# Optimization experiments

Hardware: AMD Instinct MI355X
Metric: run time of the kernel (lower is better)

Reference implementation:

```python
import jax, jax.numpy as jnp
import numpy as np

B, S, H = 4, 2048, 1024
NH, HD = 16, 64  # num heads, head dim
SCALE = 1.0 / np.sqrt(HD).astype(np.float32)
CLAMP = 1e9
EPS = 1e-9

def setup_inputs() -> dict:
    key = jax.random.key(0)
    ks = jax.random.split(key, 4)
    w_std = 0.02
    return {
        "hidden_states": jax.random.normal(ks[0], (B, S, H), dtype=jnp.float32),
        "Wq": jax.random.normal(ks[1], (H, H), dtype=jnp.float32) * w_std,
        "bq": jnp.zeros((H,), dtype=jnp.float32),
        "Wk": jax.random.normal(ks[2], (H, H), dtype=jnp.float32) * w_std,
        "bk": jnp.zeros((H,), dtype=jnp.float32),
        "Wv": jax.random.normal(ks[3], (H, H), dtype=jnp.float32) * w_std,
        "bv": jnp.zeros((H,), dtype=jnp.float32),
    }

def reference(hidden_states, Wq, bq, Wk, bk, Wv, bv):
    b, s, h = hidden_states.shape
    # linear projections, then split heads: [B,S,H] -> [B,S,NH,HD]
    q = (hidden_states @ Wq + bq).reshape(b, s, NH, HD)
    k = (hidden_states @ Wk + bk).reshape(b, s, NH, HD)
    v = (hidden_states @ Wv + bv).reshape(b, s, NH, HD)
    # scores: [B,NH,Sq,Sk]
    scores = jnp.einsum("bqhd,bkhd->bhqk", q, k) * SCALE
    scores = jnp.clip(scores, -CLAMP, CLAMP)
    probs = jax.nn.softmax(scores, axis=-1) + EPS
    # dropout: eval mode (identity)
    ctx = jnp.einsum("bhqk,bkhd->bqhd", probs, v)
    return ctx.reshape(b, s, h)
```

## Files before the change

### kernel.cpp

```cpp
#include <hip/hip_runtime.h>
#include <hip/hip_bf16.h>
#include <stdint.h>

#define B_ 4
#define S_ 2048
#define H_ 1024
#define NH_ 16
#define HD_ 64
#define SCALE_ 0.125f
#define LOG2E_ 1.4426950408889634f

typedef __bf16 bf16x8 __attribute__((ext_vector_type(8)));
typedef float f32x4 __attribute__((ext_vector_type(4)));
typedef unsigned short us4 __attribute__((ext_vector_type(4)));
typedef unsigned short us8 __attribute__((ext_vector_type(8)));
typedef unsigned short ushort_t;

__device__ __forceinline__ ushort_t f2bf(float f) {
  union { float f; uint32_t u; } a; a.f = f;
  uint32_t r = (a.u + 0x7fffu + ((a.u >> 16) & 1u)) >> 16;
  return (ushort_t)r;
}

__device__ __forceinline__ void async16(const void* g, void* l) {
  __builtin_amdgcn_global_load_lds(
      (const __attribute__((address_space(1))) unsigned int*)(uintptr_t)g,
      (__attribute__((address_space(3))) unsigned int*)(uintptr_t)l, 16, 0, 0);
}

__global__ __launch_bounds__(256) void conv_x(const float4* __restrict__ x,
                                              ushort_t* __restrict__ xb) {
  int i = blockIdx.x * 256 + threadIdx.x;
  float4 v = x[i];
  us4 o;
  o.x = f2bf(v.x); o.y = f2bf(v.y); o.z = f2bf(v.z); o.w = f2bf(v.w);
  *(us4*)(xb + (size_t)i * 4) = o;
}

__global__ __launch_bounds__(256) void conv_w(const float* __restrict__ Wq,
                                              const float* __restrict__ Wk,
                                              const float* __restrict__ Wv,
                                              ushort_t* __restrict__ Wt) {
  __shared__ __align__(16) ushort_t T[64 * 64];
  int bid = blockIdx.x;
  int w = bid >> 8;
  int t2 = bid & 255;
  int kt = (t2 >> 4) * 64, nt = (t2 & 15) * 64;
  const float* W = (w == 0) ? Wq : (w == 1) ? Wk : Wv;
  int tid = threadIdx.x;
  int k = tid >> 2, nq = tid & 3;
#pragma unroll
  for (int j4 = 0; j4 < 4; ++j4) {
    int n = nq * 4 + j4 * 16;
    float4 f = *(const float4*)(W + (size_t)(kt + k) * H_ + nt + n);
    us4 o;
    o.x = f2bf(f.x); o.y = f2bf(f.y); o.z = f2bf(f.z); o.w = f2bf(f.w);
    *(us4*)(T + k * 64 + (((n >> 3) ^ (k & 7)) * 8) + (n & 7)) = o;
  }
  __syncthreads();
  int n2 = tid >> 2, kq = tid & 3;
  us8 o0, o1;
#pragma unroll
  for (int j = 0; j < 16; ++j) {
    int kk = kq * 16 + j;
    ushort_t v = T[kk * 64 + (((n2 >> 3) ^ (kk & 7)) * 8) + (n2 & 7)];
    if (j < 8) o0[j] = v; else o1[j - 8] = v;
  }
  size_t obase = (size_t)w * (H_ * H_) + (size_t)(nt + n2) * H_ + kt + kq * 16;
  *(us8*)(Wt + obase) = o0;
  *(us8*)(Wt + obase + 8) = o1;
}

__global__ __launch_bounds__(256) void qkv_gemm(const ushort_t* __restrict__ Xb,
                                                const ushort_t* __restrict__ Wt,
                                                const float* __restrict__ bq,
                                                const float* __restrict__ bk,
                                                const float* __restrict__ bv,
                                                ushort_t* __restrict__ QKV) {
  __shared__ __align__(16) ushort_t As[128 * 32];
  __shared__ __align__(16) ushort_t Bs[128 * 32];
  int nb = blockIdx.x;
  int mb = blockIdx.y;
  int w = nb >> 3;
  int n_base = (nb & 7) * 128;
  int m_base = mb * 128;
  const ushort_t* Wtw = Wt + (size_t)w * (H_ * H_);
  int tid = threadIdx.x;
  int lane = tid & 63, wave = tid >> 6;
  int wr = wave >> 1, wc = wave & 1;
  int g = lane >> 4, l15 = lane & 15;

  f32x4 acc[4][4];
#pragma unroll
  for (int i = 0; i < 4; i++)
#pragma unroll
    for (int j = 0; j < 4; j++) acc[i][j] = (f32x4){0.f, 0.f, 0.f, 0.f};

  for (int kt = 0; kt < 32; ++kt) {
    int k0 = kt * 32;
    __syncthreads();
#pragma unroll
    for (int it = 0; it < 2; ++it) {
      int chunk = tid + it * 256;
      int r = chunk >> 2, c = chunk & 3;
      async16(Xb + (size_t)(m_base + r) * H_ + k0 + c * 8, As + chunk * 8);
      async16(Wtw + (size_t)(n_base + r) * H_ + k0 + c * 8, Bs + chunk * 8);
    }
    __builtin_amdgcn_s_waitcnt(0);
    __syncthreads();

    bf16x8 af[4], bf[4];
#pragma unroll
    for (int mi = 0; mi < 4; mi++)
      af[mi] = *(const bf16x8*)(As + (wr * 64 + mi * 16 + l15) * 32 + g * 8);
#pragma unroll
    for (int ni = 0; ni < 4; ni++)
      bf[ni] = *(const bf16x8*)(Bs + (wc * 64 + ni * 16 + l15) * 32 + g * 8);
#pragma unroll
    for (int mi = 0; mi < 4; mi++)
#pragma unroll
      for (int ni = 0; ni < 4; ni++)
        acc[mi][ni] = __builtin_amdgcn_mfma_f32_16x16x32_bf16(af[mi], bf[ni], acc[mi][ni], 0, 0, 0);
  }

  const float* bias = (w == 0) ? bq : (w == 1) ? bk : bv;
  float mult = (w == 0) ? SCALE_ * LOG2E_ : 1.0f;
  ushort_t* out = QKV + (size_t)w * (8192u * 1024u);
#pragma unroll
  for (int ni = 0; ni < 4; ++ni) {
    int n_col = n_base + wc * 64 + ni * 16 + l15;
    float bb = bias[n_col];
#pragma unroll
    for (int mi = 0; mi < 4; ++mi) {
      int m_row = m_base + wr * 64 + mi * 16 + g * 4;
#pragma unroll
      for (int reg = 0; reg < 4; ++reg) {
        float v = (acc[mi][ni][reg] + bb) * mult;
        out[(size_t)(m_row + reg) * H_ + n_col] = f2bf(v);
      }
    }
  }
}

__global__ __launch_bounds__(256) void transpose_v(const ushort_t* __restrict__ V,
                                                   ushort_t* __restrict__ Vt) {
  __shared__ __align__(16) ushort_t T[64 * 64];
  int st = blockIdx.x;
  int bh = blockIdx.y;
  int b = bh >> 4, h = bh & 15;
  int tid = threadIdx.x;
  int r = tid >> 3, c8 = tid & 7;
#pragma unroll
  for (int it = 0; it < 2; ++it) {
    int s = it * 32 + r;
    us8 v = *(const us8*)(V + (size_t)(b * S_ + st * 64 + s) * H_ + h * HD_ + c8 * 8);
    *(us8*)(T + s * 64 + ((c8 ^ ((s >> 3) & 7)) * 8)) = v;
  }
  __syncthreads();
#pragma unroll
  for (int it = 0; it < 2; ++it) {
    int d = it * 32 + r;
    us8 o;
#pragma unroll
    for (int j = 0; j < 8; ++j) {
      int s = c8 * 8 + j;
      o[j] = T[s * 64 + (((d >> 3) ^ c8) * 8) + (d & 7)];
    }
    *(us8*)(Vt + (size_t)(bh * 64 + d) * S_ + st * 64 + c8 * 8) = o;
  }
}

__global__ __launch_bounds__(512) void attn(const ushort_t* __restrict__ QKV,
                                            const ushort_t* __restrict__ Vt,
                                            float* __restrict__ out) {
  __shared__ __align__(16) ushort_t Ks[2][64 * 64];
  __shared__ __align__(16) ushort_t Vs[2][64 * 64];
  __shared__ __align__(16) ushort_t Ps[8][32 * 64];
  int qt = blockIdx.x;
  int bh = blockIdx.y;
  int b = bh >> 4, h = bh & 15;
  int tid = threadIdx.x, lane = tid & 63, wave = tid >> 6;
  int g = lane >> 4, l15 = lane & 15;

  const ushort_t* Qb = QKV;
  const ushort_t* Kb = QKV + 8388608u;

  bf16x8 qf[2][2];
#pragma unroll
  for (int mi = 0; mi < 2; ++mi) {
    int q_row = qt * 256 + wave * 32 + mi * 16 + l15;
    size_t qoff = (size_t)(b * S_ + q_row) * H_ + h * HD_;
    qf[mi][0] = *(const bf16x8*)(Qb + qoff + g * 8);
    qf[mi][1] = *(const bf16x8*)(Qb + qoff + 32 + g * 8);
  }

  f32x4 of[2][4], lsum[2];
#pragma unroll
  for (int mi = 0; mi < 2; mi++) {
    lsum[mi] = (f32x4){0.f, 0.f, 0.f, 0.f};
#pragma unroll
    for (int ni = 0; ni < 4; ni++) of[mi][ni] = (f32x4){0.f, 0.f, 0.f, 0.f};
  }

  union { us8 u; bf16x8 b; } uo;
#pragma unroll
  for (int j = 0; j < 8; ++j) uo.u[j] = 0x3F80;
  bf16x8 ones = uo.b;

  ushort_t* Pw = Ps[wave];
  int swz = l15 & 7;

  int s0 = tid >> 3;
  int cg0 = (tid & 7) ^ (s0 & 7);
  const ushort_t* srcK = Kb + (size_t)(b * S_ + s0) * H_ + h * HD_ + cg0 * 8;
  const ushort_t* srcV = Vt + ((size_t)bh * 64 + s0) * S_ + cg0 * 8;

  async16(srcK, Ks[0] + tid * 8);
  async16(srcV, Vs[0] + tid * 8);

#pragma unroll 2
  for (int kb = 0; kb < 32; ++kb) {
    int cur = kb & 1, nxt = cur ^ 1;
    __syncthreads();
    if (kb < 31) {
      async16(srcK + (size_t)(kb + 1) * 64 * H_, Ks[nxt] + tid * 8);
      async16(srcV + (size_t)(kb + 1) * 64, Vs[nxt] + tid * 8);
      __builtin_amdgcn_s_waitcnt(0xF72);
    } else {
      __builtin_amdgcn_s_waitcnt(0xF70);
    }
    __syncthreads();
    const ushort_t* Kc = Ks[cur];
    const ushort_t* Vc = Vs[cur];

#pragma unroll
    for (int c = 0; c < 4; ++c) {
      int row = c * 16 + l15;
      bf16x8 k0 = *(const bf16x8*)(Kc + row * 64 + ((g ^ (row & 7)) * 8));
      bf16x8 k1 = *(const bf16x8*)(Kc + row * 64 + (((4 + g) ^ (row & 7)) * 8));
#pragma unroll
      for (int mi = 0; mi < 2; ++mi) {
        f32x4 s = (f32x4){0.f, 0.f, 0.f, 0.f};
        s = __builtin_amdgcn_mfma_f32_16x16x32_bf16(k0, qf[mi][0], s, 0, 0, 0);
        s = __builtin_amdgcn_mfma_f32_16x16x32_bf16(k1, qf[mi][1], s, 0, 0, 0);
        us4 pk;
#pragma unroll
        for (int r = 0; r < 4; ++r)
          pk[r] = (ushort_t)(__float_as_uint(exp2f(s[r])) >> 16);
        *(us4*)(Pw + (mi * 16 + l15) * 64 +
                (((c * 2 + (g >> 1)) ^ swz) * 8) + (g & 1) * 4) = pk;
      }
    }

#pragma unroll
    for (int ks = 0; ks < 2; ++ks) {
      bf16x8 p0 = *(const bf16x8*)(Pw + l15 * 64 + (((ks * 4 + g) ^ swz) * 8));
      bf16x8 p1 = *(const bf16x8*)(Pw + (16 + l15) * 64 + (((ks * 4 + g) ^ swz) * 8));
      lsum[0] = __builtin_amdgcn_mfma_f32_16x16x32_bf16(ones, p0, lsum[0], 0, 0, 0);
      lsum[1] = __builtin_amdgcn_mfma_f32_16x16x32_bf16(ones, p1, lsum[1], 0, 0, 0);
#pragma unroll
      for (int ni = 0; ni < 4; ++ni) {
        int row = ni * 16 + l15;
        bf16x8 v = *(const bf16x8*)(Vc + row * 64 + (((ks * 4 + g) ^ (row & 7)) * 8));
        of[0][ni] = __builtin_amdgcn_mfma_f32_16x16x32_bf16(v, p0, of[0][ni], 0, 0, 0);
        of[1][ni] = __builtin_amdgcn_mfma_f32_16x16x32_bf16(v, p1, of[1][ni], 0, 0, 0);
      }
    }
  }

#pragma unroll
  for (int mi = 0; mi < 2; ++mi) {
    float inv = 1.0f / lsum[mi][0];
    int qglob = qt * 256 + wave * 32 + mi * 16 + l15;
    float* obase = out + (size_t)(b * S_ + qglob) * H_ + h * HD_ + g * 4;
#pragma unroll
    for (int ni = 0; ni < 4; ++ni) {
      float4 vv;
      vv.x = of[mi][ni][0] * inv;
      vv.y = of[mi][ni][1] * inv;
      vv.z = of[mi][ni][2] * inv;
      vv.w = of[mi][ni][3] * inv;
      *(float4*)(obase + ni * 16) = vv;
    }
  }
}

extern "C" void kernel_launch(void* const* d_in, const int* in_sizes, int n_in,
                              void* d_out, int out_size, void* d_ws, size_t ws_size,
                              hipStream_t stream) {
  const float* hs = (const float*)d_in[0];
  const float* Wq = (const float*)d_in[1];
  const float* bq = (const float*)d_in[2];
  const float* Wk = (const float*)d_in[3];
  const float* bk = (const float*)d_in[4];
  const float* Wv = (const float*)d_in[5];
  const float* bv = (const float*)d_in[6];
  float* out = (float*)d_out;

  ushort_t* Xb  = (ushort_t*)d_ws;
  ushort_t* Wt  = Xb + 8388608u;
  ushort_t* QKV = Wt + 3145728u;
  ushort_t* Vtp = Xb;

  conv_x<<<8192, 256, 0, stream>>>((const float4*)hs, Xb);
  conv_w<<<768, 256, 0, stream>>>(Wq, Wk, Wv, Wt);
  qkv_gemm<<<dim3(24, 64), 256, 0, stream>>>(Xb, Wt, bq, bk, bv, QKV);
  transpose_v<<<dim3(32, 64), 256, 0, stream>>>(QKV + 16777216u, Vtp);
  attn<<<dim3(8, 64), 512, 0, stream>>>(QKV, Vtp, out);
}
```

Before: 273.0 us.

## Fuse V transpose into QKV GEMM epilogue and widen attention waves to 64 rows

The QKV GEMM now writes V directly in head-transposed layout, which removes the separate transpose kernel and its extra global round trip. The attention kernel moves to 4 waves per block, each handling 64 query rows, so every K/V fragment read from LDS feeds twice as many MFMAs. The row sum is now accumulated in fp32 on the VALU with a cross-lane shuffle instead of extra ones-vector MFMAs. Probabilities are packed with round-to-nearest via perm, and exp2 uses the hardware builtin. The risks are higher register pressure and strided 8-byte V stores in the GEMM epilogue.

```diff
diff --git a/kernel.cpp b/kernel.cpp
--- a/kernel.cpp
+++ b/kernel.cpp
@@ -14,6 +14,7 @@
 typedef float f32x4 __attribute__((ext_vector_type(4)));
 typedef unsigned short us4 __attribute__((ext_vector_type(4)));
 typedef unsigned short us8 __attribute__((ext_vector_type(8)));
+typedef unsigned int uint2_t __attribute__((ext_vector_type(2)));
 typedef unsigned short ushort_t;
 
 __device__ __forceinline__ ushort_t f2bf(float f) {
@@ -125,57 +126,48 @@
 
   const float* bias = (w == 0) ? bq : (w == 1) ? bk : bv;
   float mult = (w == 0) ? SCALE_ * LOG2E_ : 1.0f;
-  ushort_t* out = QKV + (size_t)w * (8192u * 1024u);
-#pragma unroll
-  for (int ni = 0; ni < 4; ++ni) {
-    int n_col = n_base + wc * 64 + ni * 16 + l15;
-    float bb = bias[n_col];
-#pragma unroll
-    for (int mi = 0; mi < 4; ++mi) {
-      int m_row = m_base + wr * 64 + mi * 16 + g * 4;
-#pragma unroll
-      for (int reg = 0; reg < 4; ++reg) {
-        float v = (acc[mi][ni][reg] + bb) * mult;
-        out[(size_t)(m_row + reg) * H_ + n_col] = f2bf(v);
+  if (w == 2) {
+    ushort_t* Vout = QKV + 16777216u;
+#pragma unroll
+    for (int ni = 0; ni < 4; ++ni) {
+      int n_col = n_base + wc * 64 + ni * 16 + l15;
+      float bb = bias[n_col];
+      int hh = n_col >> 6, d = n_col & 63;
+#pragma unroll
+      for (int mi = 0; mi < 4; ++mi) {
+        int m_row = m_base + wr * 64 + mi * 16 + g * 4;
+        int bbi = m_row >> 11, s = m_row & 2047;
+        us4 o;
+#pragma unroll
+        for (int reg = 0; reg < 4; ++reg) o[reg] = f2bf(acc[mi][ni][reg] + bb);
+        *(us4*)(Vout + ((size_t)((bbi * 16 + hh) * 64 + d)) * 2048 + s) = o;
       }
     }
-  }
-}
-
-__global__ __launch_bounds__(256) void transpose_v(const ushort_t* __restrict__ V,
-                                                   ushort_t* __restrict__ Vt) {
-  __shared__ __align__(16) ushort_t T[64 * 64];
-  int st = blockIdx.x;
-  int bh = blockIdx.y;
-  int b = bh >> 4, h = bh & 15;
-  int tid = threadIdx.x;
-  int r = tid >> 3, c8 = tid & 7;
-#pragma unroll
-  for (int it = 0; it < 2; ++it) {
-    int s = it * 32 + r;
-    us8 v = *(const us8*)(V + (size_t)(b * S_ + st * 64 + s) * H_ + h * HD_ + c8 * 8);
-    *(us8*)(T + s * 64 + ((c8 ^ ((s >> 3) & 7)) * 8)) = v;
-  }
-  __syncthreads();
-#pragma unroll
-  for (int it = 0; it < 2; ++it) {
-    int d = it * 32 + r;
-    us8 o;
-#pragma unroll
-    for (int j = 0; j < 8; ++j) {
-      int s = c8 * 8 + j;
-      o[j] = T[s * 64 + (((d >> 3) ^ c8) * 8) + (d & 7)];
-    }
-    *(us8*)(Vt + (size_t)(bh * 64 + d) * S_ + st * 64 + c8 * 8) = o;
-  }
-}
-
-__global__ __launch_bounds__(512) void attn(const ushort_t* __restrict__ QKV,
-                                            const ushort_t* __restrict__ Vt,
-                                            float* __restrict__ out) {
+  } else {
+    ushort_t* out = QKV + (size_t)w * (8192u * 1024u);
+#pragma unroll
+    for (int ni = 0; ni < 4; ++ni) {
+      int n_col = n_base + wc * 64 + ni * 16 + l15;
+      float bb = bias[n_col];
+#pragma unroll
+      for (int mi = 0; mi < 4; ++mi) {
+        int m_row = m_base + wr * 64 + mi * 16 + g * 4;
+#pragma unroll
+        for (int reg = 0; reg < 4; ++reg) {
+          float v = (acc[mi][ni][reg] + bb) * mult;
+          out[(size_t)(m_row + reg) * H_ + n_col] = f2bf(v);
+        }
+      }
+    }
+  }
+}
+
+__global__ __launch_bounds__(256, 2) void attn(const ushort_t* __restrict__ QKV,
+                                               const ushort_t* __restrict__ Vt,
+                                               float* __restrict__ out) {
   __shared__ __align__(16) ushort_t Ks[2][64 * 64];
   __shared__ __align__(16) ushort_t Vs[2][64 * 64];
-  __shared__ __align__(16) ushort_t Ps[8][32 * 64];
+  __shared__ __align__(16) ushort_t Ps[4][64 * 64];
   int qt = blockIdx.x;
   int bh = blockIdx.y;
   int b = bh >> 4, h = bh & 15;
@@ -185,47 +177,49 @@
   const ushort_t* Qb = QKV;
   const ushort_t* Kb = QKV + 8388608u;
 
-  bf16x8 qf[2][2];
-#pragma unroll
-  for (int mi = 0; mi < 2; ++mi) {
-    int q_row = qt * 256 + wave * 32 + mi * 16 + l15;
+  bf16x8 qf[4][2];
+#pragma unroll
+  for (int mi = 0; mi < 4; ++mi) {
+    int q_row = qt * 256 + wave * 64 + mi * 16 + l15;
     size_t qoff = (size_t)(b * S_ + q_row) * H_ + h * HD_;
     qf[mi][0] = *(const bf16x8*)(Qb + qoff + g * 8);
     qf[mi][1] = *(const bf16x8*)(Qb + qoff + 32 + g * 8);
   }
 
-  f32x4 of[2][4], lsum[2];
-#pragma unroll
-  for (int mi = 0; mi < 2; mi++) {
-    lsum[mi] = (f32x4){0.f, 0.f, 0.f, 0.f};
+  f32x4 of[4][4];
+  float lsum[4];
+#pragma unroll
+  for (int mi = 0; mi < 4; mi++) {
+    lsum[mi] = 0.f;
 #pragma unroll
     for (int ni = 0; ni < 4; ni++) of[mi][ni] = (f32x4){0.f, 0.f, 0.f, 0.f};
   }
-
-  union { us8 u; bf16x8 b; } uo;
-#pragma unroll
-  for (int j = 0; j < 8; ++j) uo.u[j] = 0x3F80;
-  bf16x8 ones = uo.b;
 
   ushort_t* Pw = Ps[wave];
   int swz = l15 & 7;
 
-  int s0 = tid >> 3;
-  int cg0 = (tid & 7) ^ (s0 & 7);
-  const ushort_t* srcK = Kb + (size_t)(b * S_ + s0) * H_ + h * HD_ + cg0 * 8;
-  const ushort_t* srcV = Vt + ((size_t)bh * 64 + s0) * S_ + cg0 * 8;
-
-  async16(srcK, Ks[0] + tid * 8);
-  async16(srcV, Vs[0] + tid * 8);
-
-#pragma unroll 2
+  int ch0 = tid, ch1 = tid + 256;
+  int s0 = ch0 >> 3, cg0 = (ch0 & 7) ^ (s0 & 7);
+  int s1 = ch1 >> 3, cg1 = (ch1 & 7) ^ (s1 & 7);
+  const ushort_t* srcK0 = Kb + (size_t)(b * S_ + s0) * H_ + h * HD_ + cg0 * 8;
+  const ushort_t* srcK1 = Kb + (size_t)(b * S_ + s1) * H_ + h * HD_ + cg1 * 8;
+  const ushort_t* srcV0 = Vt + ((size_t)bh * 64 + s0) * S_ + cg0 * 8;
+  const ushort_t* srcV1 = Vt + ((size_t)bh * 64 + s1) * S_ + cg1 * 8;
+
+  async16(srcK0, Ks[0] + ch0 * 8);
+  async16(srcK1, Ks[0] + ch1 * 8);
+  async16(srcV0, Vs[0] + ch0 * 8);
+  async16(srcV1, Vs[0] + ch1 * 8);
+
   for (int kb = 0; kb < 32; ++kb) {
     int cur = kb & 1, nxt = cur ^ 1;
     __syncthreads();
     if (kb < 31) {
-      async16(srcK + (size_t)(kb + 1) * 64 * H_, Ks[nxt] + tid * 8);
-      async16(srcV + (size_t)(kb + 1) * 64, Vs[nxt] + tid * 8);
-      __builtin_amdgcn_s_waitcnt(0xF72);
+      async16(srcK0 + (size_t)(kb + 1) * 64 * H_, Ks[nxt] + ch0 * 8);
+      async16(srcK1 + (size_t)(kb + 1) * 64 * H_, Ks[nxt] + ch1 * 8);
+      async16(srcV0 + (size_t)(kb + 1) * 64, Vs[nxt] + ch0 * 8);
+      async16(srcV1 + (size_t)(kb + 1) * 64, Vs[nxt] + ch1 * 8);
+      __builtin_amdgcn_s_waitcnt(0xF74);
     } else {
       __builtin_amdgcn_s_waitcnt(0xF70);
     }
@@ -239,39 +233,49 @@
       bf16x8 k0 = *(const bf16x8*)(Kc + row * 64 + ((g ^ (row & 7)) * 8));
       bf16x8 k1 = *(const bf16x8*)(Kc + row * 64 + (((4 + g) ^ (row & 7)) * 8));
 #pragma unroll
-      for (int mi = 0; mi < 2; ++mi) {
+      for (int mi = 0; mi < 4; ++mi) {
         f32x4 s = (f32x4){0.f, 0.f, 0.f, 0.f};
         s = __builtin_amdgcn_mfma_f32_16x16x32_bf16(k0, qf[mi][0], s, 0, 0, 0);
         s = __builtin_amdgcn_mfma_f32_16x16x32_bf16(k1, qf[mi][1], s, 0, 0, 0);
-        us4 pk;
-#pragma unroll
-        for (int r = 0; r < 4; ++r)
-          pk[r] = (ushort_t)(__float_as_uint(exp2f(s[r])) >> 16);
-        *(us4*)(Pw + (mi * 16 + l15) * 64 +
-                (((c * 2 + (g >> 1)) ^ swz) * 8) + (g & 1) * 4) = pk;
+        float p0 = __builtin_amdgcn_exp2f(s[0]);
+        float p1 = __builtin_amdgcn_exp2f(s[1]);
+        float p2 = __builtin_amdgcn_exp2f(s[2]);
+        float p3 = __builtin_amdgcn_exp2f(s[3]);
+        lsum[mi] += (p0 + p1) + (p2 + p3);
+        uint2_t pk;
+        pk.x = __builtin_amdgcn_perm(__float_as_uint(p1) + 0x8000u,
+                                     __float_as_uint(p0) + 0x8000u, 0x07060302u);
+        pk.y = __builtin_amdgcn_perm(__float_as_uint(p3) + 0x8000u,
+                                     __float_as_uint(p2) + 0x8000u, 0x07060302u);
+        *(uint2_t*)(Pw + (mi * 16 + l15) * 64 +
+                    (((c * 2 + (g >> 1)) ^ swz) * 8) + (g & 1) * 4) = pk;
       }
     }
 
 #pragma unroll
     for (int ks = 0; ks < 2; ++ks) {
-      bf16x8 p0 = *(const bf16x8*)(Pw + l15 * 64 + (((ks * 4 + g) ^ swz) * 8));
-      bf16x8 p1 = *(const bf16x8*)(Pw + (16 + l15) * 64 + (((ks * 4 + g) ^ swz) * 8));
-      lsum[0] = __builtin_amdgcn_mfma_f32_16x16x32_bf16(ones, p0, lsum[0], 0, 0, 0);
-      lsum[1] = __builtin_amdgcn_mfma_f32_16x16x32_bf16(ones, p1, lsum[1], 0, 0, 0);
+      bf16x8 pf[4];
+#pragma unroll
+      for (int mi = 0; mi < 4; ++mi)
+        pf[mi] = *(const bf16x8*)(Pw + (mi * 16 + l15) * 64 + (((ks * 4 + g) ^ swz) * 8));
 #pragma unroll
       for (int ni = 0; ni < 4; ++ni) {
         int row = ni * 16 + l15;
         bf16x8 v = *(const bf16x8*)(Vc + row * 64 + (((ks * 4 + g) ^ (row & 7)) * 8));
-        of[0][ni] = __builtin_amdgcn_mfma_f32_16x16x32_bf16(v, p0, of[0][ni], 0, 0, 0);
-        of[1][ni] = __builtin_amdgcn_mfma_f32_16x16x32_bf16(v, p1, of[1][ni], 0, 0, 0);
+#pragma unroll
+        for (int mi = 0; mi < 4; ++mi)
+          of[mi][ni] = __builtin_amdgcn_mfma_f32_16x16x32_bf16(v, pf[mi], of[mi][ni], 0, 0, 0);
       }
     }
   }
 
 #pragma unroll
-  for (int mi = 0; mi < 2; ++mi) {
-    float inv = 1.0f / lsum[mi][0];
-    int qglob = qt * 256 + wave * 32 + mi * 16 + l15;
+  for (int mi = 0; mi < 4; ++mi) {
+    float t = lsum[mi];
+    t += __shfl_xor(t, 16, 64);
+    t += __shfl_xor(t, 32, 64);
+    float inv = 1.0f / t;
+    int qglob = qt * 256 + wave * 64 + mi * 16 + l15;
     float* obase = out + (size_t)(b * S_ + qglob) * H_ + h * HD_ + g * 4;
 #pragma unroll
     for (int ni = 0; ni < 4; ++ni) {
@@ -300,11 +304,10 @@
   ushort_t* Xb  = (ushort_t*)d_ws;
   ushort_t* Wt  = Xb + 8388608u;
   ushort_t* QKV = Wt + 3145728u;
-  ushort_t* Vtp = Xb;
+  ushort_t* Vtp = QKV + 16777216u;
 
   conv_x<<<8192, 256, 0, stream>>>((const float4*)hs, Xb);
   conv_w<<<768, 256, 0, stream>>>(Wq, Wk, Wv, Wt);
   qkv_gemm<<<dim3(24, 64), 256, 0, stream>>>(Xb, Wt, bq, bk, bv, QKV);
-  transpose_v<<<dim3(32, 64), 256, 0, stream>>>(QKV + 16777216u, Vtp);
-  attn<<<dim3(8, 64), 512, 0, stream>>>(QKV, Vtp, out);
-}
+  attn<<<dim3(8, 64), 256, 0, stream>>>(QKV, Vtp, out);
+}
```

After: 262.1 us. 1.04x faster.
